# Kernel optimization log

Measured on AMD Instinct MI355X. Metric: run time of the kernel, lower is better.

The kernel has to match this reference:

```python
import jax, jax.numpy as jnp
import numpy as np

GAMMA = 1.0        # softmin temperature (module default)
BANDWIDTH = 1024.0 # Sakoe-Chiba band half-width (module default float(1024))
WARP = 0.0         # extra penalty on non-diagonal (insert/delete) moves
BIG = 1e10         # finite stand-in for +inf (safe under logsumexp/vjp)
B, N, M, DF = 32, 512, 512, 64


def _softdtw(X, Y, X_len, Y_len):
    """Soft-DTW via anti-diagonal wavefront scan.

    R[i, j] = D[i-1, j-1] + softmin_gamma(R[i-1,j-1], R[i-1,j]+warp, R[i,j-1]+warp)
    with R[0,0]=0, borders = +inf; loss[b] = R[X_len[b], Y_len[b]].
    Cells on anti-diagonal d = i+j depend only on diagonals d-1 and d-2,
    so we scan over d carrying the last two diagonals, each stored as a
    vector over i in [0, N] (vectorized over batch and diagonal cells).
    """
    Bb, Nn, _ = X.shape
    Mm = Y.shape[1]
    # Squared-Euclidean cost matrix [B, N, M]
    D = (jnp.sum(X * X, -1)[:, :, None]
         + jnp.sum(Y * Y, -1)[:, None, :]
         - 2.0 * jnp.einsum('bnd,bmd->bnm', X, Y))

    ii = jnp.arange(Nn + 1)                               # row index along diagonal
    r2 = jnp.full((Bb, Nn + 1), BIG, jnp.float32).at[:, 0].set(0.0)  # diag d=0: R[0,0]=0
    r1 = jnp.full((Bb, Nn + 1), BIG, jnp.float32)                    # diag d=1: all inf

    def step(carry, dd):
        r2, r1 = carry
        jj = dd - ii                                      # column index j = d - i
        valid = (ii >= 1) & (jj >= 1) & (jj <= Mm) & (jnp.abs(ii - jj) <= BANDWIDTH)
        Dd = D[:, jnp.clip(ii - 1, 0, Nn - 1), jnp.clip(jj - 1, 0, Mm - 1)]  # [B, N+1]
        big_col = jnp.full((Bb, 1), BIG, jnp.float32)
        r2_im1 = jnp.concatenate([big_col, r2[:, :-1]], 1)  # R[i-1, j-1]
        r1_im1 = jnp.concatenate([big_col, r1[:, :-1]], 1)  # R[i-1, j]
        z = jnp.stack([r2_im1, r1_im1 + WARP, r1 + WARP], 0)
        soft = -GAMMA * jax.nn.logsumexp(-z / GAMMA, axis=0)  # softmin
        cur = jnp.where(valid[None, :], Dd + soft, BIG)
        return (r1, cur), cur

    _, diags = jax.lax.scan(step, (r2, r1), jnp.arange(2, Nn + Mm + 1))
    # diags[k] holds anti-diagonal d = k + 2, so R[i, j] = diags[i + j - 2][:, i]
    b = jnp.arange(Bb)
    return diags[X_len + Y_len - 2, b, X_len]


def setup_inputs() -> dict:
    key = jax.random.key(0)
    k1, k2, k3, k4 = jax.random.split(key, 4)
    X = jax.random.normal(k1, (B, N, DF), jnp.float32)
    Y = jax.random.normal(k2, (B, M, DF), jnp.float32)
    X_len = jax.random.randint(k3, (B,), 3 * N // 4, N + 1).astype(jnp.int32)
    Y_len = jax.random.randint(k4, (B,), 3 * M // 4, M + 1).astype(jnp.int32)
    return {"X": X, "Y": Y, "X_len": X_len, "Y_len": Y_len}


def reference(X, Y, X_len, Y_len):
    return _softdtw(X, Y, X_len, Y_len)
```

## Files before the change

kernel.cpp:

```cpp
#include <hip/hip_runtime.h>
#include <hip/hip_fp16.h>
#include <cstddef>

#define Bc   32
#define Nc   512
#define Mc   512
#define DFc  64
#define BIGC 1.0e10f
#define LOG2E_F 1.4426950408889634f
#define LN2_F   0.6931471805599453f
#define SQRT_LOG2E_F 1.2011224087864498f

typedef unsigned int uint32;
typedef _Float16 f16x8 __attribute__((ext_vector_type(8)));
typedef float    f32x4 __attribute__((ext_vector_type(4)));

__device__ __forceinline__ float dpp_shr1(float oldv, float src) {
    return __int_as_float(__builtin_amdgcn_update_dpp(
        __float_as_int(oldv), __float_as_int(src), 0x138, 0xf, 0xf, false));
}
__device__ __forceinline__ float dpp_shr1_nc(float src) {
    return __int_as_float(__builtin_amdgcn_mov_dpp(
        __float_as_int(src), 0x138, 0xf, 0xf, false));
}
__device__ __forceinline__ float rl(float v, int lane) {
    return __int_as_float(__builtin_amdgcn_readlane(__float_as_int(v), lane));
}

__device__ __forceinline__ float softmin3m(float a, float b, float c) {
    float mn = fminf(fminf(a, b), c);
    float mx = fmaxf(fmaxf(a, b), c);
    float md = __builtin_amdgcn_fmed3f(a, b, c);
    uint32 b1 = (uint32)fmaf(mn - mx, 8388608.0f, 1065353216.0f);
    uint32 b2 = (uint32)fmaf(mn - md, 8388608.0f, 1065353216.0f);
    float E = 1.0f + (__int_as_float(b1) + __int_as_float(b2));
    return fmaf((float)__float_as_uint(E), -1.1920929e-7f, mn);
}

__global__ __launch_bounds__(256) void dist_kernel(
    const float* __restrict__ X, const float* __restrict__ Y,
    uint32* __restrict__ Dsk)
{
    __shared__ __align__(16) unsigned char SMEM[35840];
    unsigned short* XsH = (unsigned short*)SMEM;
    unsigned short* YsH = (unsigned short*)(SMEM + 16384);
    uint32* P  = (uint32*)SMEM;
    float* xx2 = (float*)(SMEM + 34816);
    float* yy2 = (float*)(SMEM + 35328);

    const int b     = blockIdx.z;
    const int strip = blockIdx.y;
    const int J     = blockIdx.x;
    const int tid   = threadIdx.x;

    const float* Xg = X + ((size_t)b * Nc + strip * 128) * DFc;
    const float* Yg = Y + ((size_t)b * Mc + J * 128) * DFc;

#pragma unroll
    for (int it = 0; it < 8; ++it) {
        int e4 = it * 256 + tid;
        int n = e4 >> 4, k4 = (e4 & 15) * 4;
        float4 v = ((const float4*)Xg)[e4];
        float sx = v.x * SQRT_LOG2E_F, sy = v.y * SQRT_LOG2E_F;
        float sz = v.z * SQRT_LOG2E_F, sw = v.w * SQRT_LOG2E_F;
        __half2 h01 = __floats2half2_rn(sx, sy);
        __half2 h23 = __floats2half2_rn(sz, sw);
        int ho = (k4 + 8 * (n & 7)) & 63;
        uint2 u; u.x = *(uint32*)&h01; u.y = *(uint32*)&h23;
        *(uint2*)&XsH[n * 64 + ho] = u;
        float p = sx * sx + sy * sy + sz * sz + sw * sw;
        p += __shfl_xor(p, 1);
        p += __shfl_xor(p, 2);
        p += __shfl_xor(p, 4);
        p += __shfl_xor(p, 8);
        if ((tid & 15) == 0) xx2[n] = p + 127.0f;
    }
#pragma unroll
    for (int it = 0; it < 8; ++it) {
        int e4 = it * 256 + tid;
        int m = e4 >> 4, k4 = (e4 & 15) * 4;
        float4 v = ((const float4*)Yg)[e4];
        float sx = v.x * SQRT_LOG2E_F, sy = v.y * SQRT_LOG2E_F;
        float sz = v.z * SQRT_LOG2E_F, sw = v.w * SQRT_LOG2E_F;
        __half2 h01 = __floats2half2_rn(sx, sy);
        __half2 h23 = __floats2half2_rn(sz, sw);
        int ho = (k4 + 8 * (m & 7)) & 63;
        uint2 u; u.x = *(uint32*)&h01; u.y = *(uint32*)&h23;
        *(uint2*)&YsH[m * 64 + ho] = u;
        float p = sx * sx + sy * sy + sz * sz + sw * sw;
        p += __shfl_xor(p, 1);
        p += __shfl_xor(p, 2);
        p += __shfl_xor(p, 4);
        p += __shfl_xor(p, 8);
        if ((tid & 15) == 0) yy2[m] = p;
    }
    __syncthreads();

    const int l  = tid & 63;
    const int w  = tid >> 6;
    const int lr = l & 15;
    const int lk = l >> 4;

    f32x4 acc[2][8];
#pragma unroll
    for (int rt = 0; rt < 2; ++rt)
#pragma unroll
        for (int ct = 0; ct < 8; ++ct) {
            f32x4 z = {0.f, 0.f, 0.f, 0.f};
            acc[rt][ct] = z;
        }

#pragma unroll
    for (int ks = 0; ks < 2; ++ks) {
        f16x8 af[2], bf[8];
#pragma unroll
        for (int rt = 0; rt < 2; ++rt) {
            int row = w * 32 + rt * 16 + lr;
            int ho = (ks * 32 + lk * 8 + 8 * (row & 7)) & 63;
            af[rt] = *(const f16x8*)&XsH[row * 64 + ho];
        }
#pragma unroll
        for (int ct = 0; ct < 8; ++ct) {
            int col = ct * 16 + lr;
            int ho = (ks * 32 + lk * 8 + 8 * (col & 7)) & 63;
            bf[ct] = *(const f16x8*)&YsH[col * 64 + ho];
        }
#pragma unroll
        for (int rt = 0; rt < 2; ++rt)
#pragma unroll
            for (int ct = 0; ct < 8; ++ct)
                acc[rt][ct] = __builtin_amdgcn_mfma_f32_16x16x32_f16(
                    af[rt], bf[ct], acc[rt][ct], 0, 0, 0);
    }
    __syncthreads();

#pragma unroll
    for (int rt = 0; rt < 2; ++rt) {
        int rbase = w * 32 + rt * 16 + 4 * lk;
        f32x4 xr = *(const f32x4*)&xx2[rbase];
        int p0 = rbase >> 1;
#pragma unroll
        for (int ct = 0; ct < 8; ++ct) {
            int c = ct * 16 + lr;
            float yv = yy2[c];
            f32x4 a = acc[rt][ct];
            float d0 = xr[0] + yv - 2.0f * a[0];
            float d1 = xr[1] + yv - 2.0f * a[1];
            float d2 = xr[2] + yv - 2.0f * a[2];
            float d3 = xr[3] + yv - 2.0f * a[3];
            __half2 h0 = __floats2half2_rn(d0, d1);
            __half2 h1 = __floats2half2_rn(d2, d3);
            P[c * 67 + p0]     = *(uint32*)&h0;
            P[c * 67 + p0 + 1] = *(uint32*)&h1;
        }
    }
    __syncthreads();

    const int q = tid >> 6;
    uint4* outt = (uint4*)Dsk + (((size_t)b * 4 + strip) * 4 + J) * 4096;
    const uint32* Pl = P + l;
#pragma unroll
    for (int gi = 0; gi < 16; ++gi) {
        int g = q + 4 * gi;
        int ka = 4 * g - 2 * l;
        int c0 = min(max(ka,     0), 127);
        int c1 = min(max(ka + 1, 0), 127);
        int c2 = min(max(ka + 2, 0), 127);
        int c3 = min(max(ka + 3, 0), 127);
        uint32 p0 = Pl[c0 * 67];
        uint32 p1 = Pl[c1 * 67];
        uint32 p2 = Pl[c2 * 67];
        uint32 p3 = Pl[c3 * 67];
        uint4 v;
        v.x = (p0 & 0xffffu) | (p1 << 16);
        v.y = (p0 >> 16)     | (p1 & 0xffff0000u);
        v.z = (p2 & 0xffffu) | (p3 << 16);
        v.w = (p2 >> 16)     | (p3 & 0xffff0000u);
        outt[g * 64 + l] = v;
    }
}

#define SSTEP(T, dAw, dBw, PH1)                                            \
  {                                                                        \
    float2 fA = __half22float2(*(const __half2*)&(dAw));                   \
    float2 fB = __half22float2(*(const __half2*)&(dBw));                   \
    float u1, u2;                                                          \
    if (PH1) {                                                             \
      u1 = dpp_shr1(rl(Fodd, (T) - 1), pub1);                              \
      u2 = dpp_shr1(rl(Fev,  (T) - 1), curB);                              \
    } else {                                                               \
      u1 = dpp_shr1_nc(pub1);                                              \
      u2 = dpp_shr1_nc(curB);                                              \
    }                                                                      \
    float A1 = softmin3m(diagA, u1, curA) + fA.x;                          \
    float A2 = softmin3m(u1, u2, A1) + fA.y;                               \
    float B1 = softmin3m(curA, A1, curB) + fB.x;                           \
    float B2 = softmin3m(A1, A2, B1) + fB.y;                               \
    if ((T) == scap)                                                       \
      capv = useB ? (useC2 ? B2 : B1) : (useC2 ? A2 : A1);                 \
    bool act = (PH1) ? (l < (T)) : (l >= (T) - 64);                        \
    pub1  = act ? B1 : curB;                 \
    curA  = act ? A2 : curA;                                               \
    curB  = act ? B2 : curB;                                               \
    diagA = u2;                                                            \
    if (!(PH1)) { wbase[2 * (T) - 127] = B1; wbase[2 * (T) - 126] = B2; }  \
  }

__global__ __launch_bounds__(256) void scan_kernel(
    const uint32* __restrict__ Dsk,
    const int* __restrict__ X_len, const int* __restrict__ Y_len,
    float* __restrict__ out)
{
    __shared__ __align__(16) float Frow[4][520];
    __shared__ float dumpArr[136];

    const int tid = threadIdx.x;
    const int l  = tid & 63;
    const int wl = __builtin_amdgcn_readfirstlane(tid >> 6);
    const int bb = blockIdx.x;

    const int xl = X_len[bb], yl = Y_len[bb];
    const int wxl  = (xl - 1) >> 7;
    const int iw   = (xl - 1) & 127;
    const int lcap = iw >> 1;
    const int useB = iw & 1;
    const int Jcap = (yl - 1) >> 7;
    const int ycol = yl - (Jcap << 7);
    const int useC2 = 1 - (ycol & 1);
    const int tcap = ((ycol + 1) >> 1) + lcap;
    const int kmax = wxl + Jcap;

    const bool is63 = (l == 63);
    const int voff = l * 16;

    const char* tbw = (const char*)Dsk +
        ((((size_t)bb * 4 + wl) * 4) * 4096) * 16;

    if (l == 0) Frow[wl][0] = BIGC;
    __syncthreads();

    float curA = BIGC, curB = BIGC, pub1 = BIGC;
    float diagA = BIGC;
    float capv = 0.0f;

    uint4 dreg[8];
    if (wl <= wxl) {
#pragma unroll
        for (int q = 0; q < 8; ++q)
            dreg[q] = *(const uint4*)(tbw + voff + q * 1024);
    }

    for (int k = 0; k <= kmax; ++k) {
        int J = k - wl;
        if (wl <= wxl && 0 <= J && J <= Jcap) {
            const int j0 = J << 7;
            float Fodd, Fev, f0;
            if (wl > 0) {
                Fodd = Frow[wl - 1][j0 + 1 + 2 * l];
                Fev  = Frow[wl - 1][j0 + 2 + 2 * l];
                f0   = Frow[wl - 1][j0];
            } else {
                Fodd = BIGC; Fev = BIGC;
                f0 = (J == 0) ? 0.0f : BIGC;
            }
            diagA = (l == 0) ? f0 : diagA;

            const char* tb = tbw + (size_t)J * 65536;
            const int scap = (wl == wxl && J == Jcap) ? tcap : -1000;
            float* wbase = is63 ? (&Frow[wl][j0]) : (dumpArr + 4);
            const bool nextJ = (J < Jcap);

#pragma unroll 1
            for (int m = 0; m < 4; ++m) {
#pragma unroll
                for (int q = 0; q < 8; ++q) {
                    const int g = m * 8 + q;
                    uint4 dc = dreg[q];
                    SSTEP(2 * g + 1, dc.x, dc.y, true)
                    SSTEP(2 * g + 2, dc.z, dc.w, true)
                    dreg[q] = *(const uint4*)(tb + voff + (g + 8) * 1024);
                }
            }
            wbase[1] = pub1;
            wbase[2] = curB;

#pragma unroll 1
            for (int m = 4; m < 7; ++m) {
#pragma unroll
                for (int q = 0; q < 8; ++q) {
                    const int g = m * 8 + q;
                    uint4 dc = dreg[q];
                    SSTEP(2 * g + 1, dc.x, dc.y, false)
                    SSTEP(2 * g + 2, dc.z, dc.w, false)
                    dreg[q] = *(const uint4*)(tb + voff + (g + 8) * 1024);
                }
            }
#pragma unroll
            for (int q = 0; q < 8; ++q) {
                const int g = 56 + q;
                uint4 dc = dreg[q];
                SSTEP(2 * g + 1, dc.x, dc.y, false)
                if (g < 63) { SSTEP(2 * g + 2, dc.z, dc.w, false) }
                if (nextJ)
                    dreg[q] = *(const uint4*)(tb + 65536 + voff + q * 1024);
            }
        }
        __syncthreads();
    }

    if (wl == wxl) {
        float o = rl(capv, lcap);
        if (l == 0) out[bb] = o * LN2_F;
    }
}

extern "C" void kernel_launch(void* const* d_in, const int* in_sizes, int n_in,
                              void* d_out, int out_size, void* d_ws, size_t ws_size,
                              hipStream_t stream)
{
    const float* X  = (const float*)d_in[0];
    const float* Y  = (const float*)d_in[1];
    const int*   xl = (const int*)d_in[2];
    const int*   yl = (const int*)d_in[3];
    float* out = (float*)d_out;
    uint32* Dsk = (uint32*)d_ws;

    dist_kernel<<<dim3(4, 4, Bc), 256, 0, stream>>>(X, Y, Dsk);
    scan_kernel<<<Bc, 256, 0, stream>>>(Dsk, xl, yl, out);
}
```

Before: 199.5 us.

## Fuse distance and scan kernels with per-tile flag synchronization

Merges the distance-matrix kernel and the wavefront scan kernel into one launch. The first 512 blocks compute distance tiles and publish a per-tile ready flag with release semantics. The last 32 blocks run the scan and spin-wait on each tile's flag before loading it. This lets the scan start while other tiles are still being computed and removes the dependency gap between launches. It adds a small init kernel to reset the flags, and correctness relies on the distance blocks being scheduled before or alongside the waiting scan blocks.

```diff
diff --git a/kernel.cpp b/kernel.cpp
--- a/kernel.cpp
+++ b/kernel.cpp
@@ -15,6 +15,8 @@
 typedef _Float16 f16x8 __attribute__((ext_vector_type(8)));
 typedef float    f32x4 __attribute__((ext_vector_type(4)));
 
+__device__ int g_flags[512];
+
 __device__ __forceinline__ float dpp_shr1(float oldv, float src) {
     return __int_as_float(__builtin_amdgcn_update_dpp(
         __float_as_int(oldv), __float_as_int(src), 0x138, 0xf, 0xf, false));
@@ -37,147 +39,15 @@
     return fmaf((float)__float_as_uint(E), -1.1920929e-7f, mn);
 }
 
-__global__ __launch_bounds__(256) void dist_kernel(
-    const float* __restrict__ X, const float* __restrict__ Y,
-    uint32* __restrict__ Dsk)
+__device__ __forceinline__ void waitflag(int* f) {
+    while (__hip_atomic_load(f, __ATOMIC_ACQUIRE, __HIP_MEMORY_SCOPE_AGENT) == 0) {
+        __builtin_amdgcn_s_sleep(2);
+    }
+}
+
+__global__ void init_kernel()
 {
-    __shared__ __align__(16) unsigned char SMEM[35840];
-    unsigned short* XsH = (unsigned short*)SMEM;
-    unsigned short* YsH = (unsigned short*)(SMEM + 16384);
-    uint32* P  = (uint32*)SMEM;
-    float* xx2 = (float*)(SMEM + 34816);
-    float* yy2 = (float*)(SMEM + 35328);
-
-    const int b     = blockIdx.z;
-    const int strip = blockIdx.y;
-    const int J     = blockIdx.x;
-    const int tid   = threadIdx.x;
-
-    const float* Xg = X + ((size_t)b * Nc + strip * 128) * DFc;
-    const float* Yg = Y + ((size_t)b * Mc + J * 128) * DFc;
-
-#pragma unroll
-    for (int it = 0; it < 8; ++it) {
-        int e4 = it * 256 + tid;
-        int n = e4 >> 4, k4 = (e4 & 15) * 4;
-        float4 v = ((const float4*)Xg)[e4];
-        float sx = v.x * SQRT_LOG2E_F, sy = v.y * SQRT_LOG2E_F;
-        float sz = v.z * SQRT_LOG2E_F, sw = v.w * SQRT_LOG2E_F;
-        __half2 h01 = __floats2half2_rn(sx, sy);
-        __half2 h23 = __floats2half2_rn(sz, sw);
-        int ho = (k4 + 8 * (n & 7)) & 63;
-        uint2 u; u.x = *(uint32*)&h01; u.y = *(uint32*)&h23;
-        *(uint2*)&XsH[n * 64 + ho] = u;
-        float p = sx * sx + sy * sy + sz * sz + sw * sw;
-        p += __shfl_xor(p, 1);
-        p += __shfl_xor(p, 2);
-        p += __shfl_xor(p, 4);
-        p += __shfl_xor(p, 8);
-        if ((tid & 15) == 0) xx2[n] = p + 127.0f;
-    }
-#pragma unroll
-    for (int it = 0; it < 8; ++it) {
-        int e4 = it * 256 + tid;
-        int m = e4 >> 4, k4 = (e4 & 15) * 4;
-        float4 v = ((const float4*)Yg)[e4];
-        float sx = v.x * SQRT_LOG2E_F, sy = v.y * SQRT_LOG2E_F;
-        float sz = v.z * SQRT_LOG2E_F, sw = v.w * SQRT_LOG2E_F;
-        __half2 h01 = __floats2half2_rn(sx, sy);
-        __half2 h23 = __floats2half2_rn(sz, sw);
-        int ho = (k4 + 8 * (m & 7)) & 63;
-        uint2 u; u.x = *(uint32*)&h01; u.y = *(uint32*)&h23;
-        *(uint2*)&YsH[m * 64 + ho] = u;
-        float p = sx * sx + sy * sy + sz * sz + sw * sw;
-        p += __shfl_xor(p, 1);
-        p += __shfl_xor(p, 2);
-        p += __shfl_xor(p, 4);
-        p += __shfl_xor(p, 8);
-        if ((tid & 15) == 0) yy2[m] = p;
-    }
-    __syncthreads();
-
-    const int l  = tid & 63;
-    const int w  = tid >> 6;
-    const int lr = l & 15;
-    const int lk = l >> 4;
-
-    f32x4 acc[2][8];
-#pragma unroll
-    for (int rt = 0; rt < 2; ++rt)
-#pragma unroll
-        for (int ct = 0; ct < 8; ++ct) {
-            f32x4 z = {0.f, 0.f, 0.f, 0.f};
-            acc[rt][ct] = z;
-        }
-
-#pragma unroll
-    for (int ks = 0; ks < 2; ++ks) {
-        f16x8 af[2], bf[8];
-#pragma unroll
-        for (int rt = 0; rt < 2; ++rt) {
-            int row = w * 32 + rt * 16 + lr;
-            int ho = (ks * 32 + lk * 8 + 8 * (row & 7)) & 63;
-            af[rt] = *(const f16x8*)&XsH[row * 64 + ho];
-        }
-#pragma unroll
-        for (int ct = 0; ct < 8; ++ct) {
-            int col = ct * 16 + lr;
-            int ho = (ks * 32 + lk * 8 + 8 * (col & 7)) & 63;
-            bf[ct] = *(const f16x8*)&YsH[col * 64 + ho];
-        }
-#pragma unroll
-        for (int rt = 0; rt < 2; ++rt)
-#pragma unroll
-            for (int ct = 0; ct < 8; ++ct)
-                acc[rt][ct] = __builtin_amdgcn_mfma_f32_16x16x32_f16(
-                    af[rt], bf[ct], acc[rt][ct], 0, 0, 0);
-    }
-    __syncthreads();
-
-#pragma unroll
-    for (int rt = 0; rt < 2; ++rt) {
-        int rbase = w * 32 + rt * 16 + 4 * lk;
-        f32x4 xr = *(const f32x4*)&xx2[rbase];
-        int p0 = rbase >> 1;
-#pragma unroll
-        for (int ct = 0; ct < 8; ++ct) {
-            int c = ct * 16 + lr;
-            float yv = yy2[c];
-            f32x4 a = acc[rt][ct];
-            float d0 = xr[0] + yv - 2.0f * a[0];
-            float d1 = xr[1] + yv - 2.0f * a[1];
-            float d2 = xr[2] + yv - 2.0f * a[2];
-            float d3 = xr[3] + yv - 2.0f * a[3];
-            __half2 h0 = __floats2half2_rn(d0, d1);
-            __half2 h1 = __floats2half2_rn(d2, d3);
-            P[c * 67 + p0]     = *(uint32*)&h0;
-            P[c * 67 + p0 + 1] = *(uint32*)&h1;
-        }
-    }
-    __syncthreads();
-
-    const int q = tid >> 6;
-    uint4* outt = (uint4*)Dsk + (((size_t)b * 4 + strip) * 4 + J) * 4096;
-    const uint32* Pl = P + l;
-#pragma unroll
-    for (int gi = 0; gi < 16; ++gi) {
-        int g = q + 4 * gi;
-        int ka = 4 * g - 2 * l;
-        int c0 = min(max(ka,     0), 127);
-        int c1 = min(max(ka + 1, 0), 127);
-        int c2 = min(max(ka + 2, 0), 127);
-        int c3 = min(max(ka + 3, 0), 127);
-        uint32 p0 = Pl[c0 * 67];
-        uint32 p1 = Pl[c1 * 67];
-        uint32 p2 = Pl[c2 * 67];
-        uint32 p3 = Pl[c3 * 67];
-        uint4 v;
-        v.x = (p0 & 0xffffu) | (p1 << 16);
-        v.y = (p0 >> 16)     | (p1 & 0xffff0000u);
-        v.z = (p2 & 0xffffu) | (p3 << 16);
-        v.w = (p2 >> 16)     | (p3 & 0xffff0000u);
-        outt[g * 64 + l] = v;
-    }
+    g_flags[threadIdx.x] = 0;
 }
 
 #define SSTEP(T, dAw, dBw, PH1)                                            \
@@ -206,18 +76,167 @@
     if (!(PH1)) { wbase[2 * (T) - 127] = B1; wbase[2 * (T) - 126] = B2; }  \
   }
 
-__global__ __launch_bounds__(256) void scan_kernel(
-    const uint32* __restrict__ Dsk,
+__global__ __launch_bounds__(256) void fused_kernel(
+    const float* __restrict__ X, const float* __restrict__ Y,
+    uint32* __restrict__ Dsk,
     const int* __restrict__ X_len, const int* __restrict__ Y_len,
     float* __restrict__ out)
 {
-    __shared__ __align__(16) float Frow[4][520];
-    __shared__ float dumpArr[136];
-
+    __shared__ __align__(16) unsigned char SMEM[35840];
+    const int bi  = blockIdx.x;
     const int tid = threadIdx.x;
+
+    if (bi < 512) {
+        unsigned short* XsH = (unsigned short*)SMEM;
+        unsigned short* YsH = (unsigned short*)(SMEM + 16384);
+        uint32* P  = (uint32*)SMEM;
+        float* xx2 = (float*)(SMEM + 34816);
+        float* yy2 = (float*)(SMEM + 35328);
+
+        const int J     = bi & 3;
+        const int strip = (bi >> 2) & 3;
+        const int b     = bi >> 4;
+
+        const float* Xg = X + ((size_t)b * Nc + strip * 128) * DFc;
+        const float* Yg = Y + ((size_t)b * Mc + J * 128) * DFc;
+
+#pragma unroll
+        for (int it = 0; it < 8; ++it) {
+            int e4 = it * 256 + tid;
+            int n = e4 >> 4, k4 = (e4 & 15) * 4;
+            float4 v = ((const float4*)Xg)[e4];
+            float sx = v.x * SQRT_LOG2E_F, sy = v.y * SQRT_LOG2E_F;
+            float sz = v.z * SQRT_LOG2E_F, sw = v.w * SQRT_LOG2E_F;
+            __half2 h01 = __floats2half2_rn(sx, sy);
+            __half2 h23 = __floats2half2_rn(sz, sw);
+            int ho = (k4 + 8 * (n & 7)) & 63;
+            uint2 u; u.x = *(uint32*)&h01; u.y = *(uint32*)&h23;
+            *(uint2*)&XsH[n * 64 + ho] = u;
+            float p = sx * sx + sy * sy + sz * sz + sw * sw;
+            p += __shfl_xor(p, 1);
+            p += __shfl_xor(p, 2);
+            p += __shfl_xor(p, 4);
+            p += __shfl_xor(p, 8);
+            if ((tid & 15) == 0) xx2[n] = p + 127.0f;
+        }
+#pragma unroll
+        for (int it = 0; it < 8; ++it) {
+            int e4 = it * 256 + tid;
+            int m = e4 >> 4, k4 = (e4 & 15) * 4;
+            float4 v = ((const float4*)Yg)[e4];
+            float sx = v.x * SQRT_LOG2E_F, sy = v.y * SQRT_LOG2E_F;
+            float sz = v.z * SQRT_LOG2E_F, sw = v.w * SQRT_LOG2E_F;
+            __half2 h01 = __floats2half2_rn(sx, sy);
+            __half2 h23 = __floats2half2_rn(sz, sw);
+            int ho = (k4 + 8 * (m & 7)) & 63;
+            uint2 u; u.x = *(uint32*)&h01; u.y = *(uint32*)&h23;
+            *(uint2*)&YsH[m * 64 + ho] = u;
+            float p = sx * sx + sy * sy + sz * sz + sw * sw;
+            p += __shfl_xor(p, 1);
+            p += __shfl_xor(p, 2);
+            p += __shfl_xor(p, 4);
+            p += __shfl_xor(p, 8);
+            if ((tid & 15) == 0) yy2[m] = p;
+        }
+        __syncthreads();
+
+        const int l  = tid & 63;
+        const int w  = tid >> 6;
+        const int lr = l & 15;
+        const int lk = l >> 4;
+
+        f32x4 acc[2][8];
+#pragma unroll
+        for (int rt = 0; rt < 2; ++rt)
+#pragma unroll
+            for (int ct = 0; ct < 8; ++ct) {
+                f32x4 z = {0.f, 0.f, 0.f, 0.f};
+                acc[rt][ct] = z;
+            }
+
+#pragma unroll
+        for (int ks = 0; ks < 2; ++ks) {
+            f16x8 af[2], bf[8];
+#pragma unroll
+            for (int rt = 0; rt < 2; ++rt) {
+                int row = w * 32 + rt * 16 + lr;
+                int ho = (ks * 32 + lk * 8 + 8 * (row & 7)) & 63;
+                af[rt] = *(const f16x8*)&XsH[row * 64 + ho];
+            }
+#pragma unroll
+            for (int ct = 0; ct < 8; ++ct) {
+                int col = ct * 16 + lr;
+                int ho = (ks * 32 + lk * 8 + 8 * (col & 7)) & 63;
+                bf[ct] = *(const f16x8*)&YsH[col * 64 + ho];
+            }
+#pragma unroll
+            for (int rt = 0; rt < 2; ++rt)
+#pragma unroll
+                for (int ct = 0; ct < 8; ++ct)
+                    acc[rt][ct] = __builtin_amdgcn_mfma_f32_16x16x32_f16(
+                        af[rt], bf[ct], acc[rt][ct], 0, 0, 0);
+        }
+        __syncthreads();
+
+#pragma unroll
+        for (int rt = 0; rt < 2; ++rt) {
+            int rbase = w * 32 + rt * 16 + 4 * lk;
+            f32x4 xr = *(const f32x4*)&xx2[rbase];
+            int p0 = rbase >> 1;
+#pragma unroll
+            for (int ct = 0; ct < 8; ++ct) {
+                int c = ct * 16 + lr;
+                float yv = yy2[c];
+                f32x4 a = acc[rt][ct];
+                float d0 = xr[0] + yv - 2.0f * a[0];
+                float d1 = xr[1] + yv - 2.0f * a[1];
+                float d2 = xr[2] + yv - 2.0f * a[2];
+                float d3 = xr[3] + yv - 2.0f * a[3];
+                __half2 h0 = __floats2half2_rn(d0, d1);
+                __half2 h1 = __floats2half2_rn(d2, d3);
+                P[c * 67 + p0]     = *(uint32*)&h0;
+                P[c * 67 + p0 + 1] = *(uint32*)&h1;
+            }
+        }
+        __syncthreads();
+
+        const int q = tid >> 6;
+        uint4* outt = (uint4*)Dsk + (((size_t)b * 4 + strip) * 4 + J) * 4096;
+        const uint32* Pl = P + l;
+#pragma unroll
+        for (int gi = 0; gi < 16; ++gi) {
+            int g = q + 4 * gi;
+            int ka = 4 * g - 2 * l;
+            int c0 = min(max(ka,     0), 127);
+            int c1 = min(max(ka + 1, 0), 127);
+            int c2 = min(max(ka + 2, 0), 127);
+            int c3 = min(max(ka + 3, 0), 127);
+            uint32 p0 = Pl[c0 * 67];
+            uint32 p1 = Pl[c1 * 67];
+            uint32 p2 = Pl[c2 * 67];
+            uint32 p3 = Pl[c3 * 67];
+            uint4 v;
+            v.x = (p0 & 0xffffu) | (p1 << 16);
+            v.y = (p0 >> 16)     | (p1 & 0xffff0000u);
+            v.z = (p2 & 0xffffu) | (p3 << 16);
+            v.w = (p2 >> 16)     | (p3 & 0xffff0000u);
+            outt[g * 64 + l] = v;
+        }
+
+        __threadfence();
+        __syncthreads();
+        if (tid == 0)
+            __hip_atomic_store(&g_flags[(b * 4 + strip) * 4 + J], 1,
+                               __ATOMIC_RELEASE, __HIP_MEMORY_SCOPE_AGENT);
+        return;
+    }
+
+    float* FrowP   = (float*)SMEM;
+    float* dumpP   = (float*)(SMEM + 8320);
+
     const int l  = tid & 63;
     const int wl = __builtin_amdgcn_readfirstlane(tid >> 6);
-    const int bb = blockIdx.x;
+    const int bb = bi - 512;
 
     const int xl = X_len[bb], yl = Y_len[bb];
     const int wxl  = (xl - 1) >> 7;
@@ -235,8 +254,9 @@
 
     const char* tbw = (const char*)Dsk +
         ((((size_t)bb * 4 + wl) * 4) * 4096) * 16;
-
-    if (l == 0) Frow[wl][0] = BIGC;
+    int* fbase = &g_flags[(bb * 4 + wl) * 4];
+
+    if (l == 0) FrowP[wl * 520] = BIGC;
     __syncthreads();
 
     float curA = BIGC, curB = BIGC, pub1 = BIGC;
@@ -245,6 +265,7 @@
 
     uint4 dreg[8];
     if (wl <= wxl) {
+        waitflag(fbase);
 #pragma unroll
         for (int q = 0; q < 8; ++q)
             dreg[q] = *(const uint4*)(tbw + voff + q * 1024);
@@ -256,9 +277,9 @@
             const int j0 = J << 7;
             float Fodd, Fev, f0;
             if (wl > 0) {
-                Fodd = Frow[wl - 1][j0 + 1 + 2 * l];
-                Fev  = Frow[wl - 1][j0 + 2 + 2 * l];
-                f0   = Frow[wl - 1][j0];
+                Fodd = FrowP[(wl - 1) * 520 + j0 + 1 + 2 * l];
+                Fev  = FrowP[(wl - 1) * 520 + j0 + 2 + 2 * l];
+                f0   = FrowP[(wl - 1) * 520 + j0];
             } else {
                 Fodd = BIGC; Fev = BIGC;
                 f0 = (J == 0) ? 0.0f : BIGC;
@@ -267,7 +288,7 @@
 
             const char* tb = tbw + (size_t)J * 65536;
             const int scap = (wl == wxl && J == Jcap) ? tcap : -1000;
-            float* wbase = is63 ? (&Frow[wl][j0]) : (dumpArr + 4);
+            float* wbase = is63 ? (&FrowP[wl * 520 + j0]) : (dumpP + 4);
             const bool nextJ = (J < Jcap);
 
 #pragma unroll 1
@@ -295,6 +316,7 @@
                     dreg[q] = *(const uint4*)(tb + voff + (g + 8) * 1024);
                 }
             }
+            if (nextJ) waitflag(fbase + J + 1);
 #pragma unroll
             for (int q = 0; q < 8; ++q) {
                 const int g = 56 + q;
@@ -325,6 +347,6 @@
     float* out = (float*)d_out;
     uint32* Dsk = (uint32*)d_ws;
 
-    dist_kernel<<<dim3(4, 4, Bc), 256, 0, stream>>>(X, Y, Dsk);
-    scan_kernel<<<Bc, 256, 0, stream>>>(Dsk, xl, yl, out);
-}
+    init_kernel<<<1, 512, 0, stream>>>();
+    fused_kernel<<<544, 256, 0, stream>>>(X, Y, Dsk, xl, yl, out);
+}
```

Result: slower. 273.2 us (+36.9%).

## Restructure soft-DTW scan into fine-grained 16-step blocks with ring-buffer wave handoff

Applied to the files above, without the earlier changes.

Each wave's strip is now traversed as one continuous skewed diagonal stream over the whole row, instead of per 128-column tile. Waves hand off boundary values through a small 64-entry LDS ring buffer and synchronize every 16 steps with a fixed 80-step lag between waves. The pipeline fill is therefore shorter than the old one-tile-per-wave stagger, and the per-step readlane of the previous wave's row is gone. The distance kernel is changed to write the matching row-contiguous skewed layout, with partial edge stores. In exchange there are many more __syncthreads barriers, and correctness depends on the ring buffer not being overwritten before the next wave reads it.

```diff
diff --git a/kernel.cpp b/kernel.cpp
--- a/kernel.cpp
+++ b/kernel.cpp
@@ -18,10 +18,6 @@
 __device__ __forceinline__ float dpp_shr1(float oldv, float src) {
     return __int_as_float(__builtin_amdgcn_update_dpp(
         __float_as_int(oldv), __float_as_int(src), 0x138, 0xf, 0xf, false));
-}
-__device__ __forceinline__ float dpp_shr1_nc(float src) {
-    return __int_as_float(__builtin_amdgcn_mov_dpp(
-        __float_as_int(src), 0x138, 0xf, 0xf, false));
 }
 __device__ __forceinline__ float rl(float v, int lane) {
     return __int_as_float(__builtin_amdgcn_readlane(__float_as_int(v), lane));
@@ -156,54 +152,67 @@
     }
     __syncthreads();
 
-    const int q = tid >> 6;
-    uint4* outt = (uint4*)Dsk + (((size_t)b * 4 + strip) * 4 + J) * 4096;
-    const uint32* Pl = P + l;
-#pragma unroll
-    for (int gi = 0; gi < 16; ++gi) {
-        int g = q + 4 * gi;
-        int ka = 4 * g - 2 * l;
-        int c0 = min(max(ka,     0), 127);
-        int c1 = min(max(ka + 1, 0), 127);
-        int c2 = min(max(ka + 2, 0), 127);
-        int c3 = min(max(ka + 3, 0), 127);
-        uint32 p0 = Pl[c0 * 67];
-        uint32 p1 = Pl[c1 * 67];
-        uint32 p2 = Pl[c2 * 67];
-        uint32 p3 = Pl[c3 * 67];
-        uint4 v;
-        v.x = (p0 & 0xffffu) | (p1 << 16);
-        v.y = (p0 >> 16)     | (p1 & 0xffff0000u);
-        v.z = (p2 & 0xffffu) | (p3 << 16);
-        v.w = (p2 >> 16)     | (p3 & 0xffff0000u);
-        outt[g * 64 + l] = v;
-    }
-}
-
-#define SSTEP(T, dAw, dBw, PH1)                                            \
+    {
+        char* rbp = (char*)Dsk + (size_t)((b * 4 + strip) * 262144);
+        const int q = tid >> 6;
+        const int lpar = l & 1;
+        const int nfull = 32 - lpar;
+        const int pbase = 32 * J + ((l + lpar) >> 1);
+        for (int k = q; k < nfull; k += 4) {
+            int p = pbase + k;
+            int tc0 = 4 * k + 2 * lpar;
+            uint32 p0 = P[(tc0    ) * 67 + l];
+            uint32 p1 = P[(tc0 + 1) * 67 + l];
+            uint32 p2 = P[(tc0 + 2) * 67 + l];
+            uint32 p3 = P[(tc0 + 3) * 67 + l];
+            uint4 v;
+            v.x = (p0 & 0xffffu) | (p1 << 16);
+            v.y = (p0 >> 16)     | (p1 & 0xffff0000u);
+            v.z = (p2 & 0xffffu) | (p3 << 16);
+            v.w = (p2 >> 16)     | (p3 & 0xffff0000u);
+            *(uint4*)(rbp + p * 1024 + l * 16) = v;
+        }
+        if (lpar && q == 3) {
+            int pL = 32 * J + ((l - 1) >> 1);
+            uint32 a0 = P[0 * 67 + l], a1 = P[1 * 67 + l];
+            uint2 u;
+            u.x = (a0 & 0xffffu) | (a1 << 16);
+            u.y = (a0 >> 16)     | (a1 & 0xffff0000u);
+            *(uint2*)(rbp + pL * 1024 + l * 16 + 8) = u;
+            int pR = 32 * J + 31 + ((l + 1) >> 1);
+            uint32 b0 = P[126 * 67 + l], b1 = P[127 * 67 + l];
+            uint2 w2;
+            w2.x = (b0 & 0xffffu) | (b1 << 16);
+            w2.y = (b0 >> 16)     | (b1 & 0xffff0000u);
+            *(uint2*)(rbp + pR * 1024 + l * 16) = w2;
+        }
+    }
+}
+
+#define NSTEP(J_, dAw, dBw)                                                \
   {                                                                        \
+    float u1 = dpp_shr1(evO[J_], pub1);                                    \
+    float u2 = dpp_shr1(evE[J_], curB);                                    \
     float2 fA = __half22float2(*(const __half2*)&(dAw));                   \
     float2 fB = __half22float2(*(const __half2*)&(dBw));                   \
-    float u1, u2;                                                          \
-    if (PH1) {                                                             \
-      u1 = dpp_shr1(rl(Fodd, (T) - 1), pub1);                              \
-      u2 = dpp_shr1(rl(Fev,  (T) - 1), curB);                              \
-    } else {                                                               \
-      u1 = dpp_shr1_nc(pub1);                                              \
-      u2 = dpp_shr1_nc(curB);                                              \
-    }                                                                      \
     float A1 = softmin3m(diagA, u1, curA) + fA.x;                          \
     float A2 = softmin3m(u1, u2, A1) + fA.y;                               \
     float B1 = softmin3m(curA, A1, curB) + fB.x;                           \
     float B2 = softmin3m(A1, A2, B1) + fB.y;                               \
-    if ((T) == scap)                                                       \
+    if (ls0 + (J_) == scap)                                                \
       capv = useB ? (useC2 ? B2 : B1) : (useC2 ? A2 : A1);                 \
-    bool act = (PH1) ? (l < (T)) : (l >= (T) - 64);                        \
-    pub1  = act ? B1 : curB;                 \
-    curA  = act ? A2 : curA;                                               \
-    curB  = act ? B2 : curB;                                               \
+    {                                                                      \
+      int c = ls0 + (J_) - l;                                              \
+      bool act = ((unsigned)c <= 255u);                                    \
+      pub1  = act ? B1 : curB;               \
+      curA  = act ? A2 : curA;                                             \
+      curB  = act ? B2 : curB;                                             \
+    }                                                                      \
     diagA = u2;                                                            \
-    if (!(PH1)) { wbase[2 * (T) - 127] = B1; wbase[2 * (T) - 126] = B2; }  \
+    {                                                                      \
+      float* wbs = pubEdge ? &ering[wl][(ls0 + (J_) + 1) & 63][0] : dumpw; \
+      wbs[0] = B1; wbs[1] = B2;                                            \
+    }                                                                      \
   }
 
 __global__ __launch_bounds__(256) void scan_kernel(
@@ -211,104 +220,71 @@
     const int* __restrict__ X_len, const int* __restrict__ Y_len,
     float* __restrict__ out)
 {
-    __shared__ __align__(16) float Frow[4][520];
-    __shared__ float dumpArr[136];
+    __shared__ __align__(16) float ering[4][64][2];
+    __shared__ float dumpw[4];
 
     const int tid = threadIdx.x;
-    const int l  = tid & 63;
-    const int wl = __builtin_amdgcn_readfirstlane(tid >> 6);
-    const int bb = blockIdx.x;
+    const int l   = tid & 63;
+    const int wl  = __builtin_amdgcn_readfirstlane(tid >> 6);
+    const int bb  = blockIdx.x;
 
     const int xl = X_len[bb], yl = Y_len[bb];
-    const int wxl  = (xl - 1) >> 7;
-    const int iw   = (xl - 1) & 127;
-    const int lcap = iw >> 1;
-    const int useB = iw & 1;
-    const int Jcap = (yl - 1) >> 7;
-    const int ycol = yl - (Jcap << 7);
-    const int useC2 = 1 - (ycol & 1);
-    const int tcap = ((ycol + 1) >> 1) + lcap;
-    const int kmax = wxl + Jcap;
-
-    const bool is63 = (l == 63);
+    const int gcap = (xl - 1) >> 1;
+    const int wcap = gcap >> 6;
+    const int lcap = gcap & 63;
+    const int useB  = (xl - 1) & 1;
+    const int useC2 = (yl - 1) & 1;
+    const int ccap  = (yl - 1) >> 1;
+    const int scapw = ccap + lcap;
+    const int scap  = (wl == wcap) ? scapw : -1000;
+    const int blkmax = (80 * wcap + scapw) >> 4;
+
+    const char* tbw = (const char*)Dsk + (size_t)((bb * 4 + wl) * 262144);
     const int voff = l * 16;
-
-    const char* tbw = (const char*)Dsk +
-        ((((size_t)bb * 4 + wl) * 4) * 4096) * 16;
-
-    if (l == 0) Frow[wl][0] = BIGC;
-    __syncthreads();
+    const bool pubEdge = (l == 63) && (wl < 3);
 
     float curA = BIGC, curB = BIGC, pub1 = BIGC;
-    float diagA = BIGC;
+    float diagA = (wl == 0 && l == 0) ? 0.0f : BIGC;
     float capv = 0.0f;
 
     uint4 dreg[8];
-    if (wl <= wxl) {
-#pragma unroll
-        for (int q = 0; q < 8; ++q)
-            dreg[q] = *(const uint4*)(tbw + voff + q * 1024);
-    }
-
-    for (int k = 0; k <= kmax; ++k) {
-        int J = k - wl;
-        if (wl <= wxl && 0 <= J && J <= Jcap) {
-            const int j0 = J << 7;
-            float Fodd, Fev, f0;
+#pragma unroll
+    for (int q = 0; q < 8; ++q)
+        dreg[q] = *(const uint4*)(tbw + q * 1024 + voff);
+
+    for (int blk = 0; blk <= blkmax; ++blk) {
+        const int ls0 = blk * 16 - 80 * wl;
+        if (wl <= wcap && 0 <= ls0 && ls0 <= 304) {
+            float evO[16], evE[16];
             if (wl > 0) {
-                Fodd = Frow[wl - 1][j0 + 1 + 2 * l];
-                Fev  = Frow[wl - 1][j0 + 2 + 2 * l];
-                f0   = Frow[wl - 1][j0];
+                const float* rb = &ering[wl - 1][ls0 & 63][0];
+#pragma unroll
+                for (int j = 0; j < 16; j += 2) {
+                    float4 t = *(const float4*)(rb + 2 * j);
+                    bool v0 = (ls0 + j)     <= 255;
+                    bool v1 = (ls0 + j + 1) <= 255;
+                    evO[j]     = v0 ? t.x : BIGC;
+                    evE[j]     = v0 ? t.y : BIGC;
+                    evO[j + 1] = v1 ? t.z : BIGC;
+                    evE[j + 1] = v1 ? t.w : BIGC;
+                }
             } else {
-                Fodd = BIGC; Fev = BIGC;
-                f0 = (J == 0) ? 0.0f : BIGC;
+#pragma unroll
+                for (int j = 0; j < 16; ++j) { evO[j] = BIGC; evE[j] = BIGC; }
             }
-            diagA = (l == 0) ? f0 : diagA;
-
-            const char* tb = tbw + (size_t)J * 65536;
-            const int scap = (wl == wxl && J == Jcap) ? tcap : -1000;
-            float* wbase = is63 ? (&Frow[wl][j0]) : (dumpArr + 4);
-            const bool nextJ = (J < Jcap);
-
-#pragma unroll 1
-            for (int m = 0; m < 4; ++m) {
-#pragma unroll
-                for (int q = 0; q < 8; ++q) {
-                    const int g = m * 8 + q;
-                    uint4 dc = dreg[q];
-                    SSTEP(2 * g + 1, dc.x, dc.y, true)
-                    SSTEP(2 * g + 2, dc.z, dc.w, true)
-                    dreg[q] = *(const uint4*)(tb + voff + (g + 8) * 1024);
-                }
+            const char* tbB = tbw + (size_t)(ls0 >> 1) * 1024 + voff;
+#pragma unroll
+            for (int q = 0; q < 8; ++q) {
+                uint4 dc = dreg[q];
+                dreg[q] = *(const uint4*)(tbB + (q + 8) * 1024);
+                NSTEP(2 * q,     dc.x, dc.y)
+                NSTEP(2 * q + 1, dc.z, dc.w)
             }
-            wbase[1] = pub1;
-            wbase[2] = curB;
-
-#pragma unroll 1
-            for (int m = 4; m < 7; ++m) {
-#pragma unroll
-                for (int q = 0; q < 8; ++q) {
-                    const int g = m * 8 + q;
-                    uint4 dc = dreg[q];
-                    SSTEP(2 * g + 1, dc.x, dc.y, false)
-                    SSTEP(2 * g + 2, dc.z, dc.w, false)
-                    dreg[q] = *(const uint4*)(tb + voff + (g + 8) * 1024);
-                }
-            }
-#pragma unroll
-            for (int q = 0; q < 8; ++q) {
-                const int g = 56 + q;
-                uint4 dc = dreg[q];
-                SSTEP(2 * g + 1, dc.x, dc.y, false)
-                if (g < 63) { SSTEP(2 * g + 2, dc.z, dc.w, false) }
-                if (nextJ)
-                    dreg[q] = *(const uint4*)(tb + 65536 + voff + q * 1024);
-            }
         }
         __syncthreads();
     }
 
-    if (wl == wxl) {
+    if (wl == wcap) {
         float o = rl(capv, lcap);
         if (l == 0) out[bb] = o * LN2_F;
     }
```

Result: faster. 168.6 us (-15.5%).
